# Kernel optimization log

Hardware: AMD Instinct MI355X
Metric: run time of the kernel (lower is better)

## Reference

```python
import jax, jax.numpy as jnp
import numpy as np

B, S, C, O, H = 4, 4096, 2048, 2048, 8
DH = O // H  # per-head dim = 256
EPS = 1e-5


def setup_inputs() -> dict:
    key = jax.random.key(0)
    ks = jax.random.split(key, 12)
    init = lambda k, shape: (jax.random.normal(k, shape, dtype=jnp.float32) * 0.02)
    return {
        "x": jax.random.normal(ks[0], (B, S, C), dtype=jnp.float32),
        "Wq": init(ks[1], (C, O)), "bq": jnp.zeros((O,), jnp.float32),
        "Wk": init(ks[2], (C, O)), "bk": jnp.zeros((O,), jnp.float32),
        "Wv": init(ks[3], (C, O)), "bv": jnp.zeros((O,), jnp.float32),
        "Wo": init(ks[4], (O, C)), "bo": jnp.zeros((C,), jnp.float32),
        "gamma": jnp.ones((C,), jnp.float32),
        "beta": jnp.zeros((C,), jnp.float32),
    }


def reference(x, Wq, bq, Wk, bk, Wv, bv, Wo, bo, gamma, beta):
    b, s, _ = x.shape
    q = (x @ Wq + bq).reshape(b, s, H, DH)
    k = (x @ Wk + bk).reshape(b, s, H, DH)
    v = (x @ Wv + bv).reshape(b, s, H, DH)
    # As written in the source: matmul over the LAST two dims of [B,S,H,DH],
    # i.e. per-position attention across heads -> scores [B,S,H,H].
    scores = jnp.einsum("bshd,bstd->bsht", q, k) / jnp.sqrt(jnp.float32(DH))
    attn = jax.nn.softmax(scores, axis=-1)
    attended = jnp.einsum("bsht,bstd->bshd", attn, v).reshape(b, s, O)
    out = attended @ Wo + bo
    # residual + LayerNorm over the channel dim
    y = x + out
    mu = jnp.mean(y, axis=-1, keepdims=True)
    var = jnp.mean(jnp.square(y - mu), axis=-1, keepdims=True)
    return gamma * (y - mu) * jax.lax.rsqrt(var + EPS) + beta
```

## Files before the change

kernel.cpp:

```cpp
#include <hip/hip_runtime.h>
#include <hip/hip_bf16.h>
#include <stdint.h>


using short8  = __attribute__((ext_vector_type(8))) short;
using floatx4 = __attribute__((ext_vector_type(4))) float;

__device__ __forceinline__ float bf2f(ushort u) {
    union { uint32_t i; float f; } v; v.i = ((uint32_t)u) << 16; return v.f;
}
__device__ __forceinline__ ushort f2bf(float f) {
    union { float f; uint32_t i; } v; v.f = f;
    uint32_t r = v.i + 0x7fffu + ((v.i >> 16) & 1u);
    return (ushort)(r >> 16);
}
__device__ __forceinline__ short8 pack8(const floatx4& a, const floatx4& b) {
    short8 o;
    o[0] = (short)f2bf(a[0]); o[1] = (short)f2bf(a[1]);
    o[2] = (short)f2bf(a[2]); o[3] = (short)f2bf(a[3]);
    o[4] = (short)f2bf(b[0]); o[5] = (short)f2bf(b[1]);
    o[6] = (short)f2bf(b[2]); o[7] = (short)f2bf(b[3]);
    return o;
}
__device__ __forceinline__ void async_copy16(const void* g, void* l) {
    __builtin_amdgcn_global_load_lds(
        (__attribute__((address_space(1))) uint32_t*)g,
        (__attribute__((address_space(3))) uint32_t*)l,
        16, 0, 0);
}

#define GBAR do { asm volatile("" ::: "memory"); \
                  __builtin_amdgcn_s_barrier(); \
                  asm volatile("" ::: "memory"); } while (0)
#define LGKM0 asm volatile("s_waitcnt lgkmcnt(0)" ::: "memory")

__global__ void cvt_bf16(const float* __restrict__ in, ushort* __restrict__ out) {
    const size_t base = ((size_t)blockIdx.x * 256 + threadIdx.x) * 8;
    floatx4 a = *(const floatx4*)&in[base];
    floatx4 b = *(const floatx4*)&in[base + 4];
    *(short8*)&out[base] = pack8(a, b);
}

__global__ void convT2048(const float* __restrict__ in, ushort* __restrict__ out) {
    __shared__ alignas(16) float tile[32][33];
    const int x = blockIdx.x * 32 + threadIdx.x;
    const int y0 = blockIdx.y * 32;
    for (int j = threadIdx.y; j < 32; j += 8)
        tile[j][threadIdx.x] = in[(size_t)(y0 + j) * 2048 + x];
    __syncthreads();
    const int x2 = blockIdx.y * 32 + threadIdx.x;
    const int y2 = blockIdx.x * 32;
    for (int j = threadIdx.y; j < 32; j += 8)
        out[(size_t)(y2 + j) * 2048 + x2] = f2bf(tile[threadIdx.x][j]);
}

template <typename CT, int N>
__global__ __launch_bounds__(512, 2)
void gemm256(const ushort* __restrict__ A, int lda,
             const ushort* __restrict__ Bt,
             const float* __restrict__ b0, const float* __restrict__ b1,
             const float* __restrict__ b2,
             const float* __restrict__ resid, CT* __restrict__ C)
{
    constexpr int K   = 2048;
    constexpr int NKT = K / 64;
    constexpr int NT  = N / 256;
    constexpr int SW  = NT / 8;
    __shared__ alignas(16) ushort lA[2][256 * 64];
    __shared__ alignas(16) ushort lB[2][256 * 64];

    const int t    = threadIdx.x;
    const int wid  = t >> 6, lane = t & 63;
    const int wr   = wid >> 2, wc = wid & 3;
    const int lr   = lane & 15, q4 = lane >> 4;
    const int swk  = lr & 7;

    const int l    = (int)blockIdx.x;
    const int xcd  = l & 7;
    const int j2   = l >> 3;
    const int row0 = (j2 / SW) * 256;
    const int col0 = (xcd * SW + (j2 % SW)) * 256;

    const float* bias; int boff;
    if (col0 < 2048)      { bias = b0; boff = 0; }
    else if (col0 < 4096) { bias = b1; boff = 2048; }
    else                  { bias = b2; boff = 4096; }

    const int rpb = t >> 3;
    const int sp  = t & 7;
    const int gc0 = (sp ^ (rpb & 7)) * 8;
    const ushort* pA0 = A  + (size_t)(row0 + rpb)      * lda + gc0;
    const ushort* pA1 = A  + (size_t)(row0 + 64 + rpb) * lda + gc0;
    const ushort* pB0 = Bt + (size_t)(col0 + rpb)      * K   + gc0;
    const ushort* pB1 = Bt + (size_t)(col0 + 64 + rpb) * K   + gc0;

#define STAGE_A(buf, half, kn) do { \
    async_copy16(pA0 + (size_t)(half) * 128 * lda + (kn) * 64, \
                 &lA[buf][(half) * 8192 + t * 8]); \
    async_copy16(pA1 + (size_t)(half) * 128 * lda + (kn) * 64, \
                 &lA[buf][(half) * 8192 + 4096 + t * 8]); \
} while (0)
#define STAGE_B(buf, half, kn) do { \
    async_copy16(pB0 + (size_t)(half) * 128 * K + (kn) * 64, \
                 &lB[buf][(half) * 8192 + t * 8]); \
    async_copy16(pB1 + (size_t)(half) * 128 * K + (kn) * 64, \
                 &lB[buf][(half) * 8192 + 4096 + t * 8]); \
} while (0)

    const int arow = (wr * 128 + lr) * 64;
    const int brow = (wc * 64  + lr) * 64;
    const int c0 = ((0 + q4) ^ swk) * 8;
    const int c1 = ((4 + q4) ^ swk) * 8;

    floatx4 acc[8][4];
    #pragma unroll
    for (int i = 0; i < 8; i++)
        #pragma unroll
        for (int j = 0; j < 4; j++)
            acc[i][j] = (floatx4){0.f, 0.f, 0.f, 0.f};

    STAGE_A(0, 0, 0); STAGE_A(0, 1, 0);
    STAGE_B(0, 0, 0); STAGE_B(0, 1, 0);
    STAGE_A(1, 0, 1); STAGE_A(1, 1, 1);
    asm volatile("s_waitcnt vmcnt(4)" ::: "memory");
    GBAR;

    short8 bf[4][2];
    short8 aq[4][2][2];

#define LOAD_AQ(q) do { \
    _Pragma("unroll") \
    for (int m = 0; m < 2; m++) { \
        aq[q][m][0] = *(const short8*)&lA[c][arow + ((q) * 2 + m) * 1024 + c0]; \
        aq[q][m][1] = *(const short8*)&lA[c][arow + ((q) * 2 + m) * 1024 + c1]; \
    } \
} while (0)
#define MFMA_Q(q) do { \
    _Pragma("unroll") \
    for (int m = 0; m < 2; m++) \
        _Pragma("unroll") \
        for (int j = 0; j < 4; j++) \
            _Pragma("unroll") \
            for (int ks = 0; ks < 2; ks++) \
                acc[(q) * 2 + m][j] = __builtin_amdgcn_mfma_f32_16x16x32_bf16( \
                    aq[q][m][ks], bf[j][ks], acc[(q) * 2 + m][j], 0, 0, 0); \
} while (0)

    for (int kt = 0; kt < NKT; ++kt) {
        const int c = kt & 1;

        #pragma unroll
        for (int j = 0; j < 2; j++) {
            bf[j][0] = *(const short8*)&lB[c][brow + j * 1024 + c0];
            bf[j][1] = *(const short8*)&lB[c][brow + j * 1024 + c1];
        }
        LOAD_AQ(0);
        #pragma unroll
        for (int j = 2; j < 4; j++) {
            bf[j][0] = *(const short8*)&lB[c][brow + j * 1024 + c0];
            bf[j][1] = *(const short8*)&lB[c][brow + j * 1024 + c1];
        }
        LOAD_AQ(1);
        if (kt < NKT - 1) STAGE_B(c ^ 1, 0, kt + 1);
        GBAR;
        __builtin_amdgcn_s_setprio(1);
        MFMA_Q(0);
        __builtin_amdgcn_s_setprio(0);

        LOAD_AQ(2);
        if (kt < NKT - 1) STAGE_B(c ^ 1, 1, kt + 1);
        GBAR;
        __builtin_amdgcn_s_setprio(1);
        MFMA_Q(1);
        __builtin_amdgcn_s_setprio(0);

        LOAD_AQ(3);
        GBAR;
        __builtin_amdgcn_s_setprio(1);
        MFMA_Q(2);
        __builtin_amdgcn_s_setprio(0);

        LGKM0;
        GBAR;
        if (kt < NKT - 2) { STAGE_A(c, 0, kt + 2); STAGE_A(c, 1, kt + 2); }
        __builtin_amdgcn_s_setprio(1);
        MFMA_Q(3);
        __builtin_amdgcn_s_setprio(0);
        if (kt < NKT - 2)       { asm volatile("s_waitcnt vmcnt(4)" ::: "memory"); }
        else if (kt == NKT - 2) { asm volatile("s_waitcnt vmcnt(0)" ::: "memory"); }
        if (kt < NKT - 1) GBAR;
    }
#undef STAGE_A
#undef STAGE_B
#undef LOAD_AQ
#undef MFMA_Q

    #pragma unroll
    for (int j = 0; j < 4; j++) {
        const int gcol = col0 + wc * 64 + j * 16 + lr;
        const float bv = bias[gcol - boff];
        #pragma unroll
        for (int i = 0; i < 8; i++) {
            #pragma unroll
            for (int r = 0; r < 4; r++) {
                const int grow = row0 + wr * 128 + i * 16 + q4 * 4 + r;
                const size_t off = (size_t)grow * N + gcol;
                float v = acc[i][j][r] + bv;
                if (resid) v += resid[off];
                if constexpr (__is_same(CT, float)) C[off] = v;
                else                                C[off] = f2bf(v);
            }
        }
    }
}

template <int N>
__global__ __launch_bounds__(256, 2)
void gemm_f32a(const float* __restrict__ A, int lda,
               const ushort* __restrict__ Bt,
               const float* __restrict__ b0, const float* __restrict__ b1,
               const float* __restrict__ b2, ushort* __restrict__ C)
{
    constexpr int K = 2048;
    constexpr int NT = N / 128;
    constexpr int SW = NT / 8;
    __shared__ alignas(16) float  lA32[128 * 32];
    __shared__ alignas(16) ushort lB[128 * 32];

    const int t = threadIdx.x;
    const int wave = t >> 6, lane = t & 63;

    const int l = (int)blockIdx.x;
    const int xcd = l & 7;
    const int j2 = l >> 3;
    const int row0 = (j2 / SW) * 128;
    const int col0 = (xcd * SW + (j2 % SW)) * 128;

    const float* bias; int boff;
    if (col0 < 2048)      { bias = b0; boff = 0; }
    else if (col0 < 4096) { bias = b1; boff = 2048; }
    else                  { bias = b2; boff = 4096; }

    const int ar = t >> 3, ac = (t & 7) * 4;
    const float* gA0 = A + (size_t)(row0 + ar) * lda + ac;
    const ushort* gB0 = Bt + (size_t)(col0 + (t >> 2)) * K + (t & 3) * 8;
    const ushort* gB1 = Bt + (size_t)(col0 + 64 + (t >> 2)) * K + (t & 3) * 8;

    const int wm = (wave >> 1) * 64;
    const int wn = (wave & 1) * 64;
    const int q4 = lane >> 4;
    const int lr = lane & 15;

    floatx4 acc[4][4];
    #pragma unroll
    for (int i = 0; i < 4; i++)
        #pragma unroll
        for (int j = 0; j < 4; j++)
            acc[i][j] = (floatx4){0.f, 0.f, 0.f, 0.f};

    for (int kt = 0; kt < K / 32; ++kt) {
        const int ko = kt * 32;
        #pragma unroll
        for (int n = 0; n < 4; n++)
            async_copy16(gA0 + (size_t)n * 32 * lda + ko, &lA32[(n * 256 + t) * 4]);
        async_copy16(gB0 + ko, &lB[t * 8]);
        async_copy16(gB1 + ko, &lB[2048 + t * 8]);
        __syncthreads();

        short8 af[4], bfr[4];
        #pragma unroll
        for (int i = 0; i < 4; i++) {
            const floatx4* pa = (const floatx4*)&lA32[(wm + i * 16 + lr) * 32 + q4 * 8];
            af[i] = pack8(pa[0], pa[1]);
        }
        #pragma unroll
        for (int j = 0; j < 4; j++)
            bfr[j] = *(const short8*)&lB[(wn + j * 16 + lr) * 32 + q4 * 8];

        #pragma unroll
        for (int i = 0; i < 4; i++)
            #pragma unroll
            for (int j = 0; j < 4; j++)
                acc[i][j] = __builtin_amdgcn_mfma_f32_16x16x32_bf16(
                    af[i], bfr[j], acc[i][j], 0, 0, 0);
        __syncthreads();
    }

    #pragma unroll
    for (int j = 0; j < 4; j++) {
        const int gcol = col0 + wn + j * 16 + lr;
        const float bv = bias[gcol - boff];
        #pragma unroll
        for (int i = 0; i < 4; i++)
            #pragma unroll
            for (int r = 0; r < 4; r++) {
                const int grow = row0 + wm + i * 16 + q4 * 4 + r;
                C[(size_t)grow * N + gcol] = f2bf(acc[i][j][r] + bv);
            }
    }
}

__global__ __launch_bounds__(256, 2)
void attn_kernel(ushort* __restrict__ qkv)
{
    __shared__ alignas(16) ushort sq[4][2048];
    __shared__ alignas(16) ushort sk[4][2048];
    __shared__ alignas(16) ushort sv[4][2048];
    const int wave = threadIdx.x >> 6, lane = threadIdx.x & 63;
    const size_t p = (size_t)blockIdx.x * 4 + wave;
    const size_t base = p * 6144;

    #pragma unroll
    for (int c = 0; c < 4; c++) {
        const int idx = c * 512 + lane * 8;
        *(short8*)&sq[wave][idx] = *(const short8*)&qkv[base + idx];
        *(short8*)&sk[wave][idx] = *(const short8*)&qkv[base + 2048 + idx];
        *(short8*)&sv[wave][idx] = *(const short8*)&qkv[base + 4096 + idx];
    }

    const int h = lane >> 3;
    const int tt = lane & 7;
    float s = 0.f;
    #pragma unroll 4
    for (int c = 0; c < 32; c++) {
        short8 qv = *(const short8*)&sq[wave][h * 256 + c * 8];
        short8 kv = *(const short8*)&sk[wave][tt * 256 + c * 8];
        #pragma unroll
        for (int e = 0; e < 8; e++)
            s += bf2f((ushort)qv[e]) * bf2f((ushort)kv[e]);
    }
    s *= (1.0f / 16.0f);

    float m = s;
    m = fmaxf(m, __shfl_xor(m, 1));
    m = fmaxf(m, __shfl_xor(m, 2));
    m = fmaxf(m, __shfl_xor(m, 4));
    float e = __expf(s - m);
    float sum = e;
    sum += __shfl_xor(sum, 1);
    sum += __shfl_xor(sum, 2);
    sum += __shfl_xor(sum, 4);
    const float w = e / sum;

    float wt[8];
    #pragma unroll
    for (int t2 = 0; t2 < 8; t2++)
        wt[t2] = __shfl(w, (lane & 56) + t2);

    const int d0 = (lane & 7) * 8;
    #pragma unroll
    for (int c = 0; c < 4; c++) {
        const int d = d0 + c * 64;
        float acc[8] = {0, 0, 0, 0, 0, 0, 0, 0};
        #pragma unroll
        for (int t2 = 0; t2 < 8; t2++) {
            short8 vv = *(const short8*)&sv[wave][t2 * 256 + d];
            #pragma unroll
            for (int e2 = 0; e2 < 8; e2++)
                acc[e2] += wt[t2] * bf2f((ushort)vv[e2]);
        }
        short8 o;
        #pragma unroll
        for (int e2 = 0; e2 < 8; e2++)
            o[e2] = (short)f2bf(acc[e2]);
        *(short8*)&qkv[base + h * 256 + d] = o;
    }
}

__global__ __launch_bounds__(256, 2)
void ln_kernel(float* __restrict__ y, const float* __restrict__ gamma,
               const float* __restrict__ beta)
{
    __shared__ float red[2][4];
    const int t = threadIdx.x;
    const size_t base = (size_t)blockIdx.x * 2048 + t * 8;
    floatx4 a = *(const floatx4*)&y[base];
    floatx4 b = *(const floatx4*)&y[base + 4];
    float f[8] = {a[0], a[1], a[2], a[3], b[0], b[1], b[2], b[3]};
    float s = 0.f, ss = 0.f;
    #pragma unroll
    for (int e = 0; e < 8; e++) { s += f[e]; ss += f[e] * f[e]; }
    #pragma unroll
    for (int off = 1; off < 64; off <<= 1) {
        s  += __shfl_xor(s, off);
        ss += __shfl_xor(ss, off);
    }
    const int wave = t >> 6, lane = t & 63;
    if (lane == 0) { red[0][wave] = s; red[1][wave] = ss; }
    __syncthreads();
    s  = red[0][0] + red[0][1] + red[0][2] + red[0][3];
    ss = red[1][0] + red[1][1] + red[1][2] + red[1][3];
    const float mu  = s * (1.f / 2048.f);
    const float var = fmaxf(ss * (1.f / 2048.f) - mu * mu, 0.f);
    const float rs  = rsqrtf(var + 1e-5f);
    floatx4 g0 = *(const floatx4*)&gamma[t * 8];
    floatx4 g1 = *(const floatx4*)&gamma[t * 8 + 4];
    floatx4 b0 = *(const floatx4*)&beta[t * 8];
    floatx4 b1 = *(const floatx4*)&beta[t * 8 + 4];
    floatx4 o0, o1;
    #pragma unroll
    for (int e = 0; e < 4; e++) {
        o0[e] = g0[e] * (f[e] - mu) * rs + b0[e];
        o1[e] = g1[e] * (f[e + 4] - mu) * rs + b1[e];
    }
    *(floatx4*)&y[base]     = o0;
    *(floatx4*)&y[base + 4] = o1;
}

extern "C" void kernel_launch(void* const* d_in, const int* in_sizes, int n_in,
                              void* d_out, int out_size, void* d_ws, size_t ws_size,
                              hipStream_t stream)
{
    const float* x     = (const float*)d_in[0];
    const float* Wq    = (const float*)d_in[1];
    const float* bq    = (const float*)d_in[2];
    const float* Wk    = (const float*)d_in[3];
    const float* bk    = (const float*)d_in[4];
    const float* Wv    = (const float*)d_in[5];
    const float* bv    = (const float*)d_in[6];
    const float* Wo    = (const float*)d_in[7];
    const float* bo    = (const float*)d_in[8];
    const float* gamma = (const float*)d_in[9];
    const float* beta  = (const float*)d_in[10];
    float* out = (float*)d_out;

    char* ws = (char*)d_ws;
    const size_t MB = 1024 * 1024;
    ushort* WqkvT = (ushort*)(ws + 0 * MB);
    ushort* WoT   = (ushort*)(ws + 24 * MB);

    const bool bigws = ws_size >= 288 * MB;
    ushort* xbf = (ushort*)(ws + 32 * MB);
    ushort* qkv = (ushort*)(ws + (bigws ? 96 : 32) * MB);

    dim3 tb(32, 8), tg(64, 64);
    convT2048<<<tg, tb, 0, stream>>>(Wq, WqkvT);
    convT2048<<<tg, tb, 0, stream>>>(Wk, WqkvT + 2048 * 2048);
    convT2048<<<tg, tb, 0, stream>>>(Wv, WqkvT + 2 * 2048 * 2048);
    convT2048<<<tg, tb, 0, stream>>>(Wo, WoT);

    if (bigws) {
        cvt_bf16<<<16384, 256, 0, stream>>>(x, xbf);
        gemm256<ushort, 6144><<<1536, 512, 0, stream>>>(
            xbf, 2048, WqkvT, bq, bk, bv, nullptr, qkv);
    } else {
        gemm_f32a<6144><<<6144, 256, 0, stream>>>(
            x, 2048, WqkvT, bq, bk, bv, qkv);
    }

    attn_kernel<<<4096, 256, 0, stream>>>(qkv);

    gemm256<float, 2048><<<512, 512, 0, stream>>>(
        qkv, 6144, WoT, bo, bo, bo, x, out);

    ln_kernel<<<16384, 256, 0, stream>>>(out, gamma, beta);
}
```

Before: 1.028 ms.

## Restructure GEMM main loop to prefetch next-tile LDS fragments across iterations

Reorders the double-buffered GEMM K-loop so that the B fragments and the first A quarter for the next k-tile are read from LDS during the last MFMA group of the current tile. B staging now runs two tiles ahead and A one tile ahead, with B loaded for tiles 0 and 1 in the prologue. This is meant to hide LDS read latency at the start of each iteration and drop the extra lgkmcnt wait plus one barrier. It changes the vmcnt accounting and buffer reuse ordering, so a wrong wait count could race on the LDS buffers.

```diff
diff --git a/kernel.cpp b/kernel.cpp
--- a/kernel.cpp
+++ b/kernel.cpp
@@ -32,7 +32,6 @@
 #define GBAR do { asm volatile("" ::: "memory"); \
                   __builtin_amdgcn_s_barrier(); \
                   asm volatile("" ::: "memory"); } while (0)
-#define LGKM0 asm volatile("s_waitcnt lgkmcnt(0)" ::: "memory")
 
 __global__ void cvt_bf16(const float* __restrict__ in, ushort* __restrict__ out) {
     const size_t base = ((size_t)blockIdx.x * 256 + threadIdx.x) * 8;
@@ -119,20 +118,21 @@
         for (int j = 0; j < 4; j++)
             acc[i][j] = (floatx4){0.f, 0.f, 0.f, 0.f};
 
-    STAGE_A(0, 0, 0); STAGE_A(0, 1, 0);
-    STAGE_B(0, 0, 0); STAGE_B(0, 1, 0);
-    STAGE_A(1, 0, 1); STAGE_A(1, 1, 1);
-    asm volatile("s_waitcnt vmcnt(4)" ::: "memory");
-    GBAR;
-
-    short8 bf[4][2];
+    short8 bfr[4][2];
     short8 aq[4][2][2];
 
-#define LOAD_AQ(q) do { \
+#define LOAD_AQ(q, buf) do { \
     _Pragma("unroll") \
     for (int m = 0; m < 2; m++) { \
-        aq[q][m][0] = *(const short8*)&lA[c][arow + ((q) * 2 + m) * 1024 + c0]; \
-        aq[q][m][1] = *(const short8*)&lA[c][arow + ((q) * 2 + m) * 1024 + c1]; \
+        aq[q][m][0] = *(const short8*)&lA[buf][arow + ((q) * 2 + m) * 1024 + c0]; \
+        aq[q][m][1] = *(const short8*)&lA[buf][arow + ((q) * 2 + m) * 1024 + c1]; \
+    } \
+} while (0)
+#define LOAD_B(buf) do { \
+    _Pragma("unroll") \
+    for (int j = 0; j < 4; j++) { \
+        bfr[j][0] = *(const short8*)&lB[buf][brow + j * 1024 + c0]; \
+        bfr[j][1] = *(const short8*)&lB[buf][brow + j * 1024 + c1]; \
     } \
 } while (0)
 #define MFMA_Q(q) do { \
@@ -143,56 +143,62 @@
             _Pragma("unroll") \
             for (int ks = 0; ks < 2; ks++) \
                 acc[(q) * 2 + m][j] = __builtin_amdgcn_mfma_f32_16x16x32_bf16( \
-                    aq[q][m][ks], bf[j][ks], acc[(q) * 2 + m][j], 0, 0, 0); \
+                    aq[q][m][ks], bfr[j][ks], acc[(q) * 2 + m][j], 0, 0, 0); \
 } while (0)
+
+    STAGE_A(0, 0, 0); STAGE_A(0, 1, 0);
+    STAGE_B(0, 0, 0); STAGE_B(0, 1, 0);
+    STAGE_A(1, 0, 1); STAGE_A(1, 1, 1);
+    STAGE_B(1, 0, 1); STAGE_B(1, 1, 1);
+    asm volatile("s_waitcnt vmcnt(8)" ::: "memory");
+    GBAR;
+    LOAD_B(0);
+    LOAD_AQ(0, 0);
 
     for (int kt = 0; kt < NKT; ++kt) {
         const int c = kt & 1;
 
-        #pragma unroll
-        for (int j = 0; j < 2; j++) {
-            bf[j][0] = *(const short8*)&lB[c][brow + j * 1024 + c0];
-            bf[j][1] = *(const short8*)&lB[c][brow + j * 1024 + c1];
-        }
-        LOAD_AQ(0);
-        #pragma unroll
-        for (int j = 2; j < 4; j++) {
-            bf[j][0] = *(const short8*)&lB[c][brow + j * 1024 + c0];
-            bf[j][1] = *(const short8*)&lB[c][brow + j * 1024 + c1];
-        }
-        LOAD_AQ(1);
-        if (kt < NKT - 1) STAGE_B(c ^ 1, 0, kt + 1);
+        LOAD_AQ(1, c);
         GBAR;
+        if (kt >= 1 && kt <= NKT - 2) { STAGE_A(c ^ 1, 0, kt + 1);
+                                        STAGE_A(c ^ 1, 1, kt + 1); }
         __builtin_amdgcn_s_setprio(1);
         MFMA_Q(0);
         __builtin_amdgcn_s_setprio(0);
 
-        LOAD_AQ(2);
-        if (kt < NKT - 1) STAGE_B(c ^ 1, 1, kt + 1);
+        LOAD_AQ(2, c);
         GBAR;
+        if (kt <= NKT - 3) STAGE_B(c, 0, kt + 2);
         __builtin_amdgcn_s_setprio(1);
         MFMA_Q(1);
         __builtin_amdgcn_s_setprio(0);
 
-        LOAD_AQ(3);
+        LOAD_AQ(3, c);
         GBAR;
+        if (kt <= NKT - 3) STAGE_B(c, 1, kt + 2);
         __builtin_amdgcn_s_setprio(1);
         MFMA_Q(2);
         __builtin_amdgcn_s_setprio(0);
 
-        LGKM0;
-        GBAR;
-        if (kt < NKT - 2) { STAGE_A(c, 0, kt + 2); STAGE_A(c, 1, kt + 2); }
-        __builtin_amdgcn_s_setprio(1);
-        MFMA_Q(3);
-        __builtin_amdgcn_s_setprio(0);
-        if (kt < NKT - 2)       { asm volatile("s_waitcnt vmcnt(4)" ::: "memory"); }
-        else if (kt == NKT - 2) { asm volatile("s_waitcnt vmcnt(0)" ::: "memory"); }
-        if (kt < NKT - 1) GBAR;
+        if (kt <= NKT - 2) {
+            if (kt <= NKT - 3) { asm volatile("s_waitcnt vmcnt(4)" ::: "memory"); }
+            else               { asm volatile("s_waitcnt vmcnt(0)" ::: "memory"); }
+            GBAR;
+            LOAD_AQ(0, c ^ 1);
+            __builtin_amdgcn_s_setprio(1);
+            MFMA_Q(3);
+            __builtin_amdgcn_s_setprio(0);
+            LOAD_B(c ^ 1);
+        } else {
+            __builtin_amdgcn_s_setprio(1);
+            MFMA_Q(3);
+            __builtin_amdgcn_s_setprio(0);
+        }
     }
 #undef STAGE_A
 #undef STAGE_B
 #undef LOAD_AQ
+#undef LOAD_B
 #undef MFMA_Q
 
     #pragma unroll
```

Result: slower. 1.065 ms (+3.6%).

## Stage GEMM epilogue through LDS for vectorized stores; move residual add into LayerNorm

Applied to the files above, without the earlier changes.

The GEMM epilogue now writes the accumulators into shared memory in four 64-row passes. Threads then read contiguous 8-element rows back and emit 16-byte vectorized global stores with the bias added, replacing the scattered scalar stores strided by row. The residual add of x moves out of the output GEMM into the LayerNorm kernel, which now reads x alongside y. This cuts uncoalesced store and residual-read traffic in the GEMMs, at the cost of extra barriers and LDS round trips in the epilogue.

```diff
diff --git a/kernel.cpp b/kernel.cpp
--- a/kernel.cpp
+++ b/kernel.cpp
@@ -60,7 +60,7 @@
              const ushort* __restrict__ Bt,
              const float* __restrict__ b0, const float* __restrict__ b1,
              const float* __restrict__ b2,
-             const float* __restrict__ resid, CT* __restrict__ C)
+             CT* __restrict__ C)
 {
     constexpr int K   = 2048;
     constexpr int NKT = K / 64;
@@ -119,13 +119,7 @@
         for (int j = 0; j < 4; j++)
             acc[i][j] = (floatx4){0.f, 0.f, 0.f, 0.f};
 
-    STAGE_A(0, 0, 0); STAGE_A(0, 1, 0);
-    STAGE_B(0, 0, 0); STAGE_B(0, 1, 0);
-    STAGE_A(1, 0, 1); STAGE_A(1, 1, 1);
-    asm volatile("s_waitcnt vmcnt(4)" ::: "memory");
-    GBAR;
-
-    short8 bf[4][2];
+    short8 bfr[4][2];
     short8 aq[4][2][2];
 
 #define LOAD_AQ(q) do { \
@@ -143,22 +137,28 @@
             _Pragma("unroll") \
             for (int ks = 0; ks < 2; ks++) \
                 acc[(q) * 2 + m][j] = __builtin_amdgcn_mfma_f32_16x16x32_bf16( \
-                    aq[q][m][ks], bf[j][ks], acc[(q) * 2 + m][j], 0, 0, 0); \
+                    aq[q][m][ks], bfr[j][ks], acc[(q) * 2 + m][j], 0, 0, 0); \
 } while (0)
+
+    STAGE_A(0, 0, 0); STAGE_A(0, 1, 0);
+    STAGE_B(0, 0, 0); STAGE_B(0, 1, 0);
+    STAGE_A(1, 0, 1); STAGE_A(1, 1, 1);
+    asm volatile("s_waitcnt vmcnt(4)" ::: "memory");
+    GBAR;
 
     for (int kt = 0; kt < NKT; ++kt) {
         const int c = kt & 1;
 
         #pragma unroll
         for (int j = 0; j < 2; j++) {
-            bf[j][0] = *(const short8*)&lB[c][brow + j * 1024 + c0];
-            bf[j][1] = *(const short8*)&lB[c][brow + j * 1024 + c1];
+            bfr[j][0] = *(const short8*)&lB[c][brow + j * 1024 + c0];
+            bfr[j][1] = *(const short8*)&lB[c][brow + j * 1024 + c1];
         }
         LOAD_AQ(0);
         #pragma unroll
         for (int j = 2; j < 4; j++) {
-            bf[j][0] = *(const short8*)&lB[c][brow + j * 1024 + c0];
-            bf[j][1] = *(const short8*)&lB[c][brow + j * 1024 + c1];
+            bfr[j][0] = *(const short8*)&lB[c][brow + j * 1024 + c0];
+            bfr[j][1] = *(const short8*)&lB[c][brow + j * 1024 + c1];
         }
         LOAD_AQ(1);
         if (kt < NKT - 1) STAGE_B(c ^ 1, 0, kt + 1);
@@ -195,20 +195,40 @@
 #undef LOAD_AQ
 #undef MFMA_Q
 
-    #pragma unroll
-    for (int j = 0; j < 4; j++) {
-        const int gcol = col0 + wc * 64 + j * 16 + lr;
-        const float bv = bias[gcol - boff];
-        #pragma unroll
-        for (int i = 0; i < 8; i++) {
+    float* sC = (float*)lA;
+    const int tcol = (t & 31) * 8;
+    #pragma unroll
+    for (int p = 0; p < 4; ++p) {
+        __syncthreads();
+        if (wr == (p >> 1)) {
+            const int ib = (p & 1) * 4;
             #pragma unroll
-            for (int r = 0; r < 4; r++) {
-                const int grow = row0 + wr * 128 + i * 16 + q4 * 4 + r;
-                const size_t off = (size_t)grow * N + gcol;
-                float v = acc[i][j][r] + bv;
-                if (resid) v += resid[off];
-                if constexpr (__is_same(CT, float)) C[off] = v;
-                else                                C[off] = f2bf(v);
+            for (int i2 = 0; i2 < 4; i2++)
+                #pragma unroll
+                for (int j = 0; j < 4; j++)
+                    #pragma unroll
+                    for (int r = 0; r < 4; r++)
+                        sC[(i2 * 16 + q4 * 4 + r) * 256 + wc * 64 + j * 16 + lr]
+                            = acc[ib + i2][j][r];
+        }
+        __syncthreads();
+        #pragma unroll
+        for (int r2 = 0; r2 < 4; ++r2) {
+            const int lrow = r2 * 16 + (t >> 5);
+            const int grow = row0 + p * 64 + lrow;
+            floatx4 v0 = *(const floatx4*)&sC[lrow * 256 + tcol];
+            floatx4 v1 = *(const floatx4*)&sC[lrow * 256 + tcol + 4];
+            const int gcol = col0 + tcol;
+            #pragma unroll
+            for (int e = 0; e < 4; e++) {
+                v0[e] += bias[gcol + e - boff];
+                v1[e] += bias[gcol + 4 + e - boff];
+            }
+            if constexpr (__is_same(CT, float)) {
+                *(floatx4*)&C[(size_t)grow * N + gcol]     = v0;
+                *(floatx4*)&C[(size_t)grow * N + gcol + 4] = v1;
+            } else {
+                *(short8*)&C[(size_t)grow * N + gcol] = pack8(v0, v1);
             }
         }
     }
@@ -368,15 +388,18 @@
 }
 
 __global__ __launch_bounds__(256, 2)
-void ln_kernel(float* __restrict__ y, const float* __restrict__ gamma,
-               const float* __restrict__ beta)
+void ln_kernel(float* __restrict__ y, const float* __restrict__ x,
+               const float* __restrict__ gamma, const float* __restrict__ beta)
 {
     __shared__ float red[2][4];
     const int t = threadIdx.x;
     const size_t base = (size_t)blockIdx.x * 2048 + t * 8;
-    floatx4 a = *(const floatx4*)&y[base];
-    floatx4 b = *(const floatx4*)&y[base + 4];
-    float f[8] = {a[0], a[1], a[2], a[3], b[0], b[1], b[2], b[3]};
+    floatx4 a  = *(const floatx4*)&y[base];
+    floatx4 b  = *(const floatx4*)&y[base + 4];
+    floatx4 xa = *(const floatx4*)&x[base];
+    floatx4 xb = *(const floatx4*)&x[base + 4];
+    float f[8] = {a[0] + xa[0], a[1] + xa[1], a[2] + xa[2], a[3] + xa[3],
+                  b[0] + xb[0], b[1] + xb[1], b[2] + xb[2], b[3] + xb[3]};
     float s = 0.f, ss = 0.f;
     #pragma unroll
     for (int e = 0; e < 8; e++) { s += f[e]; ss += f[e] * f[e]; }
@@ -442,7 +465,7 @@
     if (bigws) {
         cvt_bf16<<<16384, 256, 0, stream>>>(x, xbf);
         gemm256<ushort, 6144><<<1536, 512, 0, stream>>>(
-            xbf, 2048, WqkvT, bq, bk, bv, nullptr, qkv);
+            xbf, 2048, WqkvT, bq, bk, bv, qkv);
     } else {
         gemm_f32a<6144><<<6144, 256, 0, stream>>>(
             x, 2048, WqkvT, bq, bk, bv, qkv);
@@ -451,7 +474,7 @@
     attn_kernel<<<4096, 256, 0, stream>>>(qkv);
 
     gemm256<float, 2048><<<512, 512, 0, stream>>>(
-        qkv, 6144, WoT, bo, bo, bo, x, out);
-
-    ln_kernel<<<16384, 256, 0, stream>>>(out, gamma, beta);
-}
+        qkv, 6144, WoT, bo, bo, bo, out);
+
+    ln_kernel<<<16384, 256, 0, stream>>>(out, x, gamma, beta);
+}
```

Result: faster. 879.3 us (-14.4%).
